# Optimization experiments

Measured on AMD Instinct MI355X. Metric: run time of the kernel, lower is better.

Reference implementation:

```python
import jax, jax.numpy as jnp
import numpy as np

B, C, R, D = 32, 30, 196, 256
K = 20            # max_det_per_class
CONF = 0.5        # conf_threshold
IOU_THR = 0.3     # iou_threshold


def setup_inputs() -> dict:
    key = jax.random.key(0)
    k1, k2, k3 = jax.random.split(key, 3)
    return {
        "local_features": jax.random.normal(k1, (B, C, R, D), dtype=jnp.float32),
        "W_coords": jax.random.normal(k2, (4, D), dtype=jnp.float32) * 0.02,
        "b_coords": jnp.zeros((4,), jnp.float32),
        "W_pres": jax.random.normal(k3, (1, D), dtype=jnp.float32) * 0.02,
        "b_pres": jnp.zeros((1,), jnp.float32),
    }


def _grid_centers_xyxy(num_regions):
    # centers of a GxG grid in normalized coords, repeated to width 4 (xyxy)
    g = int(round(np.sqrt(num_regions)))
    assert g * g == num_regions
    c = (np.arange(g, dtype=np.float32) + 0.5) / g
    cy, cx = np.meshgrid(c, c, indexing="ij")
    centers = np.stack([cx, cy], axis=-1).reshape(-1, 2)  # [R, 2]
    return jnp.asarray(np.tile(centers, (1, 2)))          # [R, 4]


def _pairwise_iou(boxes):
    # boxes: [K, 4] xyxy -> [K, K]
    x1, y1, x2, y2 = boxes[:, 0], boxes[:, 1], boxes[:, 2], boxes[:, 3]
    area = jnp.clip(x2 - x1, 0) * jnp.clip(y2 - y1, 0)
    xx1 = jnp.maximum(x1[:, None], x1[None, :])
    yy1 = jnp.maximum(y1[:, None], y1[None, :])
    xx2 = jnp.minimum(x2[:, None], x2[None, :])
    yy2 = jnp.minimum(y2[:, None], y2[None, :])
    inter = jnp.clip(xx2 - xx1, 0) * jnp.clip(yy2 - yy1, 0)
    union = area[:, None] + area[None, :] - inter
    return inter / jnp.maximum(union, 1e-9)


def _nms_keep(boxes, valid):
    # boxes: [K, 4] already sorted by descending score; valid: [K] bool
    iou = _pairwise_iou(boxes)
    later = jnp.arange(K)

    def body(i, keep):
        sup = keep[i] & (iou[i] > IOU_THR) & (later > i)
        return keep & (~sup)

    return jax.lax.fori_loop(0, K, body, valid)


def _forward(local_features, W_coords, b_coords, W_pres, b_pres):
    # Linear heads: [B, C, R, D] -> [B, C, R, 4] and [B, C, R, 1]
    coords = jnp.einsum("bcrd,od->bcro", local_features, W_coords) + b_coords
    presence = jnp.einsum("bcrd,od->bcro", local_features, W_pres) + b_pres
    probs = jax.nn.sigmoid(presence[..., 0])  # [B, C, R]

    # predict_relative with xyxy format: add grid centers
    coords = coords + _grid_centers_xyxy(R)[None, None]

    # top-k per (image, class); top_k returns scores sorted descending
    probs_k, idx = jax.lax.top_k(probs, K)                      # [B, C, K]
    coords_k = jnp.take_along_axis(coords, idx[..., None], axis=2)  # [B, C, K, 4]

    # confidence threshold (padded mask instead of dynamic shapes)
    valid = probs_k > CONF

    # per-(image, class) greedy NMS; class shift in original => class-separable
    keep = jax.vmap(jax.vmap(_nms_keep))(coords_k, valid)       # [B, C, K] bool
    kf = keep.astype(coords_k.dtype)
    coords_out = coords_k * kf[..., None]
    probs_out = probs_k * kf
    return coords_out, probs_out, keep, presence


def reference(local_features, W_coords, b_coords, W_pres, b_pres):
    return _forward(local_features, W_coords, b_coords, W_pres, b_pres)
```

## Files before the change

kernel.cpp:

```cpp
#include <hip/hip_runtime.h>
#include <hip/hip_bf16.h>
#include <math.h>

#define BB 32
#define CC 30
#define RR 196
#define DD 256
#define KK 20
#define GG 14
#define CONF_ 0.5f
#define IOU_THR_ 0.3f

constexpr int COORDS_OFF = 0;
constexpr int PROBS_OFF  = BB * CC * KK * 4;
constexpr int KEEP_OFF   = PROBS_OFF + BB * CC * KK;
constexpr int PRES_OFF   = KEEP_OFF + BB * CC * KK;

typedef float v4f __attribute__((ext_vector_type(4)));

__device__ __forceinline__ float dot4v(v4f a, v4f b) {
    return a[0] * b[0] + a[1] * b[1] + a[2] * b[2] + a[3] * b[3];
}

#define PIN4(w) asm volatile("" : "+v"(w))

__global__ __launch_bounds__(256, 3) void fused_bbox_fit(
    const v4f*   __restrict__ lf,
    const float* __restrict__ W_coords,
    const float* __restrict__ b_coords,
    const float* __restrict__ W_pres,
    const float* __restrict__ b_pres,
    float* __restrict__ coords_out,
    float* __restrict__ probs_out,
    float* __restrict__ keep_out,
    float* __restrict__ presence_out)
{
    const int bc   = blockIdx.x;
    const int tid  = threadIdx.x;
    const int wv   = tid >> 6;
    const int lane = tid & 63;
    const int gr   = lane >> 4;
    const int o    = lane & 15;

    __shared__ float s_logit[RR];
    __shared__ v4f   s_box[RR];

    const v4f* __restrict__ Wp4 = reinterpret_cast<const v4f*>(W_pres);
    const v4f* __restrict__ Wc4 = reinterpret_cast<const v4f*>(W_coords);

    v4f wp0 = Wp4[o],       wp1 = Wp4[o + 16],      wp2 = Wp4[o + 32],      wp3 = Wp4[o + 48];
    v4f wa0 = Wc4[o],       wa1 = Wc4[o + 16],      wa2 = Wc4[o + 32],      wa3 = Wc4[o + 48];
    v4f wb0 = Wc4[64 + o],  wb1 = Wc4[80 + o],      wb2 = Wc4[96 + o],      wb3 = Wc4[112 + o];
    v4f wc0 = Wc4[128 + o], wc1 = Wc4[144 + o],     wc2 = Wc4[160 + o],     wc3 = Wc4[176 + o];
    v4f wd0 = Wc4[192 + o], wd1 = Wc4[208 + o],     wd2 = Wc4[224 + o],     wd3 = Wc4[240 + o];
    PIN4(wp0); PIN4(wp1); PIN4(wp2); PIN4(wp3);
    PIN4(wa0); PIN4(wa1); PIN4(wa2); PIN4(wa3);
    PIN4(wb0); PIN4(wb1); PIN4(wb2); PIN4(wb3);
    PIN4(wc0); PIN4(wc1); PIN4(wc2); PIN4(wc3);
    PIN4(wd0); PIN4(wd1); PIN4(wd2); PIN4(wd3);

    const float bp  = b_pres[0];
    const float bc0 = b_coords[0], bc1 = b_coords[1];
    const float bc2 = b_coords[2], bc3 = b_coords[3];

    const size_t tile  = (size_t)bc * RR;
    const v4f* __restrict__ tp = lf + tile * 64;
    const int    wbase = wv * 49;

    #pragma unroll 2
    for (int j = 0; j < 12; ++j) {
        const int r = wbase + 4 * j + gr;
        const v4f* __restrict__ rp = tp + (size_t)r * 64;

        const v4f x0 = rp[o];
        const v4f x1 = rp[o + 16];
        const v4f x2 = rp[o + 32];
        const v4f x3 = rp[o + 48];

        float ap = dot4v(x0, wp0) + dot4v(x1, wp1) + dot4v(x2, wp2) + dot4v(x3, wp3);
        float a0 = dot4v(x0, wa0) + dot4v(x1, wa1) + dot4v(x2, wa2) + dot4v(x3, wa3);
        float a1 = dot4v(x0, wb0) + dot4v(x1, wb1) + dot4v(x2, wb2) + dot4v(x3, wb3);
        float a2 = dot4v(x0, wc0) + dot4v(x1, wc1) + dot4v(x2, wc2) + dot4v(x3, wc3);
        float a3 = dot4v(x0, wd0) + dot4v(x1, wd1) + dot4v(x2, wd2) + dot4v(x3, wd3);

        #pragma unroll
        for (int off = 1; off <= 8; off <<= 1) {
            ap += __shfl_xor(ap, off);
            a0 += __shfl_xor(a0, off);
            a1 += __shfl_xor(a1, off);
            a2 += __shfl_xor(a2, off);
            a3 += __shfl_xor(a3, off);
        }
        if (o == 0) {
            const float lg = ap + bp;
            s_logit[r] = lg;
            presence_out[tile + r] = lg;
            const int   ix = r % GG, iy = r / GG;
            const float cx = (ix + 0.5f) / (float)GG;
            const float cy = (iy + 0.5f) / (float)GG;
            v4f b; b[0] = a0 + bc0 + cx; b[1] = a1 + bc1 + cy;
                   b[2] = a2 + bc2 + cx; b[3] = a3 + bc3 + cy;
            s_box[r] = b;
        }
    }

    if (gr == 0) {
        const int r = wbase + 48;
        const v4f* __restrict__ rp = tp + (size_t)r * 64;
        const v4f x0 = rp[o];
        const v4f x1 = rp[o + 16];
        const v4f x2 = rp[o + 32];
        const v4f x3 = rp[o + 48];

        float ap = dot4v(x0, wp0) + dot4v(x1, wp1) + dot4v(x2, wp2) + dot4v(x3, wp3);
        float a0 = dot4v(x0, wa0) + dot4v(x1, wa1) + dot4v(x2, wa2) + dot4v(x3, wa3);
        float a1 = dot4v(x0, wb0) + dot4v(x1, wb1) + dot4v(x2, wb2) + dot4v(x3, wb3);
        float a2 = dot4v(x0, wc0) + dot4v(x1, wc1) + dot4v(x2, wc2) + dot4v(x3, wc3);
        float a3 = dot4v(x0, wd0) + dot4v(x1, wd1) + dot4v(x2, wd2) + dot4v(x3, wd3);

        #pragma unroll
        for (int off = 1; off <= 8; off <<= 1) {
            ap += __shfl_xor(ap, off);
            a0 += __shfl_xor(a0, off);
            a1 += __shfl_xor(a1, off);
            a2 += __shfl_xor(a2, off);
            a3 += __shfl_xor(a3, off);
        }
        if (o == 0) {
            const float lg = ap + bp;
            s_logit[r] = lg;
            presence_out[tile + r] = lg;
            const int   ix = r % GG, iy = r / GG;
            const float cx = (ix + 0.5f) / (float)GG;
            const float cy = (iy + 0.5f) / (float)GG;
            v4f b; b[0] = a0 + bc0 + cx; b[1] = a1 + bc1 + cy;
                   b[2] = a2 + bc2 + cx; b[3] = a3 + bc3 + cy;
            s_box[r] = b;
        }
    }

    __syncthreads();
    if (wv != 0) return;

    float v[4]; int id[4];
    #pragma unroll
    for (int t = 0; t < 4; ++t) {
        const int r = lane + 64 * t;
        id[t] = r;
        v[t]  = (r < RR) ? s_logit[r] : -1e30f;
    }

    float myv = -1e30f; int myi = 0;
    for (int k = 0; k < KK; ++k) {
        float bv = v[0]; int bi = id[0];
        #pragma unroll
        for (int t = 1; t < 4; ++t)
            if (v[t] > bv || (v[t] == bv && id[t] < bi)) { bv = v[t]; bi = id[t]; }
        #pragma unroll
        for (int off = 32; off; off >>= 1) {
            const float ov = __shfl_xor(bv, off);
            const int   oi = __shfl_xor(bi, off);
            if (ov > bv || (ov == bv && oi < bi)) { bv = ov; bi = oi; }
        }
        #pragma unroll
        for (int t = 0; t < 4; ++t)
            if (id[t] == bi) v[t] = -1e30f;
        if (lane == k) { myv = bv; myi = bi; }
    }

    float x1 = 0.f, y1 = 0.f, x2 = 0.f, y2 = 0.f, area = 0.f, prob = 0.f;
    int kp = 0;
    if (lane < KK) {
        const v4f b = s_box[myi];
        x1 = b[0]; y1 = b[1]; x2 = b[2]; y2 = b[3];
        area = fmaxf(x2 - x1, 0.f) * fmaxf(y2 - y1, 0.f);
        prob = 1.f / (1.f + expf(-myv));
        kp   = (prob > CONF_) ? 1 : 0;
    }
    for (int i = 0; i < KK; ++i) {
        const int   ki  = __shfl(kp, i);
        const float bx1 = __shfl(x1, i), by1 = __shfl(y1, i);
        const float bx2 = __shfl(x2, i), by2 = __shfl(y2, i);
        const float ai  = __shfl(area, i);
        if (lane > i && lane < KK && ki) {
            const float xx1 = fmaxf(x1, bx1), yy1 = fmaxf(y1, by1);
            const float xx2 = fminf(x2, bx2), yy2 = fminf(y2, by2);
            const float inter = fmaxf(xx2 - xx1, 0.f) * fmaxf(yy2 - yy1, 0.f);
            const float uni   = area + ai - inter;
            const float iou   = inter / fmaxf(uni, 1e-9f);
            if (iou > IOU_THR_) kp = 0;
        }
    }

    if (lane < KK) {
        const size_t obase = (size_t)bc * KK + lane;
        const float  kf    = kp ? 1.f : 0.f;
        coords_out[obase * 4 + 0] = x1 * kf;
        coords_out[obase * 4 + 1] = y1 * kf;
        coords_out[obase * 4 + 2] = x2 * kf;
        coords_out[obase * 4 + 3] = y2 * kf;
        probs_out[obase] = prob * kf;
        keep_out[obase]  = kf;
    }
}

extern "C" void kernel_launch(void* const* d_in, const int* in_sizes, int n_in,
                              void* d_out, int out_size, void* d_ws, size_t ws_size,
                              hipStream_t stream) {
    const float* lf       = (const float*)d_in[0];
    const float* W_coords = (const float*)d_in[1];
    const float* b_coords = (const float*)d_in[2];
    const float* W_pres   = (const float*)d_in[3];
    const float* b_pres   = (const float*)d_in[4];

    float* out          = (float*)d_out;
    float* coords_out   = out + COORDS_OFF;
    float* probs_out    = out + PROBS_OFF;
    float* keep_out     = out + KEEP_OFF;
    float* presence_out = out + PRES_OFF;

    fused_bbox_fit<<<BB * CC, 256, 0, stream>>>(
        (const v4f*)lf, W_coords, b_coords, W_pres, b_pres,
        coords_out, probs_out, keep_out, presence_out);
}
```

Baseline: 53.64 us.

## Stream feature rows into double-buffered LDS via global_load_lds DMA

Replaces per-thread global vector loads with direct global-to-LDS loads into a two-stage shared buffer of 16 rows, computing the projection from LDS while the next chunk is fetched. Intent is to overlap HBM traffic with the dot-product work and reduce register pressure from in-flight loads. It adds 13 block-wide barriers and extra LDS traffic, and the wait for the async loads may serialize the stages.

```diff
diff --git a/kernel.cpp b/kernel.cpp
--- a/kernel.cpp
+++ b/kernel.cpp
@@ -24,8 +24,8 @@
 
 #define PIN4(w) asm volatile("" : "+v"(w))
 
-__global__ __launch_bounds__(256, 3) void fused_bbox_fit(
-    const v4f*   __restrict__ lf,
+__global__ __launch_bounds__(256, 3) void fused_bbox_dma(
+    const float* __restrict__ lf,
     const float* __restrict__ W_coords,
     const float* __restrict__ b_coords,
     const float* __restrict__ W_pres,
@@ -42,17 +42,18 @@
     const int gr   = lane >> 4;
     const int o    = lane & 15;
 
+    __shared__ v4f   Xb[2][16][64];
     __shared__ float s_logit[RR];
     __shared__ v4f   s_box[RR];
 
     const v4f* __restrict__ Wp4 = reinterpret_cast<const v4f*>(W_pres);
     const v4f* __restrict__ Wc4 = reinterpret_cast<const v4f*>(W_coords);
 
-    v4f wp0 = Wp4[o],       wp1 = Wp4[o + 16],      wp2 = Wp4[o + 32],      wp3 = Wp4[o + 48];
-    v4f wa0 = Wc4[o],       wa1 = Wc4[o + 16],      wa2 = Wc4[o + 32],      wa3 = Wc4[o + 48];
-    v4f wb0 = Wc4[64 + o],  wb1 = Wc4[80 + o],      wb2 = Wc4[96 + o],      wb3 = Wc4[112 + o];
-    v4f wc0 = Wc4[128 + o], wc1 = Wc4[144 + o],     wc2 = Wc4[160 + o],     wc3 = Wc4[176 + o];
-    v4f wd0 = Wc4[192 + o], wd1 = Wc4[208 + o],     wd2 = Wc4[224 + o],     wd3 = Wc4[240 + o];
+    v4f wp0 = Wp4[o],       wp1 = Wp4[o + 16],  wp2 = Wp4[o + 32],  wp3 = Wp4[o + 48];
+    v4f wa0 = Wc4[o],       wa1 = Wc4[o + 16],  wa2 = Wc4[o + 32],  wa3 = Wc4[o + 48];
+    v4f wb0 = Wc4[64 + o],  wb1 = Wc4[80 + o],  wb2 = Wc4[96 + o],  wb3 = Wc4[112 + o];
+    v4f wc0 = Wc4[128 + o], wc1 = Wc4[144 + o], wc2 = Wc4[160 + o], wc3 = Wc4[176 + o];
+    v4f wd0 = Wc4[192 + o], wd1 = Wc4[208 + o], wd2 = Wc4[224 + o], wd3 = Wc4[240 + o];
     PIN4(wp0); PIN4(wp1); PIN4(wp2); PIN4(wp3);
     PIN4(wa0); PIN4(wa1); PIN4(wa2); PIN4(wa3);
     PIN4(wb0); PIN4(wb1); PIN4(wb2); PIN4(wb3);
@@ -63,83 +64,69 @@
     const float bc0 = b_coords[0], bc1 = b_coords[1];
     const float bc2 = b_coords[2], bc3 = b_coords[3];
 
-    const size_t tile  = (size_t)bc * RR;
-    const v4f* __restrict__ tp = lf + tile * 64;
-    const int    wbase = wv * 49;
-
-    #pragma unroll 2
-    for (int j = 0; j < 12; ++j) {
-        const int r = wbase + 4 * j + gr;
-        const v4f* __restrict__ rp = tp + (size_t)r * 64;
-
-        const v4f x0 = rp[o];
-        const v4f x1 = rp[o + 16];
-        const v4f x2 = rp[o + 32];
-        const v4f x3 = rp[o + 48];
-
-        float ap = dot4v(x0, wp0) + dot4v(x1, wp1) + dot4v(x2, wp2) + dot4v(x3, wp3);
-        float a0 = dot4v(x0, wa0) + dot4v(x1, wa1) + dot4v(x2, wa2) + dot4v(x3, wa3);
-        float a1 = dot4v(x0, wb0) + dot4v(x1, wb1) + dot4v(x2, wb2) + dot4v(x3, wb3);
-        float a2 = dot4v(x0, wc0) + dot4v(x1, wc1) + dot4v(x2, wc2) + dot4v(x3, wc3);
-        float a3 = dot4v(x0, wd0) + dot4v(x1, wd1) + dot4v(x2, wd2) + dot4v(x3, wd3);
-
-        #pragma unroll
-        for (int off = 1; off <= 8; off <<= 1) {
-            ap += __shfl_xor(ap, off);
-            a0 += __shfl_xor(a0, off);
-            a1 += __shfl_xor(a1, off);
-            a2 += __shfl_xor(a2, off);
-            a3 += __shfl_xor(a3, off);
-        }
-        if (o == 0) {
-            const float lg = ap + bp;
-            s_logit[r] = lg;
-            presence_out[tile + r] = lg;
-            const int   ix = r % GG, iy = r / GG;
-            const float cx = (ix + 0.5f) / (float)GG;
-            const float cy = (iy + 0.5f) / (float)GG;
-            v4f b; b[0] = a0 + bc0 + cx; b[1] = a1 + bc1 + cy;
-                   b[2] = a2 + bc2 + cx; b[3] = a3 + bc3 + cy;
-            s_box[r] = b;
-        }
-    }
-
-    if (gr == 0) {
-        const int r = wbase + 48;
-        const v4f* __restrict__ rp = tp + (size_t)r * 64;
-        const v4f x0 = rp[o];
-        const v4f x1 = rp[o + 16];
-        const v4f x2 = rp[o + 32];
-        const v4f x3 = rp[o + 48];
-
-        float ap = dot4v(x0, wp0) + dot4v(x1, wp1) + dot4v(x2, wp2) + dot4v(x3, wp3);
-        float a0 = dot4v(x0, wa0) + dot4v(x1, wa1) + dot4v(x2, wa2) + dot4v(x3, wa3);
-        float a1 = dot4v(x0, wb0) + dot4v(x1, wb1) + dot4v(x2, wb2) + dot4v(x3, wb3);
-        float a2 = dot4v(x0, wc0) + dot4v(x1, wc1) + dot4v(x2, wc2) + dot4v(x3, wc3);
-        float a3 = dot4v(x0, wd0) + dot4v(x1, wd1) + dot4v(x2, wd2) + dot4v(x3, wd3);
-
-        #pragma unroll
-        for (int off = 1; off <= 8; off <<= 1) {
-            ap += __shfl_xor(ap, off);
-            a0 += __shfl_xor(a0, off);
-            a1 += __shfl_xor(a1, off);
-            a2 += __shfl_xor(a2, off);
-            a3 += __shfl_xor(a3, off);
-        }
-        if (o == 0) {
-            const float lg = ap + bp;
-            s_logit[r] = lg;
-            presence_out[tile + r] = lg;
-            const int   ix = r % GG, iy = r / GG;
-            const float cx = (ix + 0.5f) / (float)GG;
-            const float cy = (iy + 0.5f) / (float)GG;
-            v4f b; b[0] = a0 + bc0 + cx; b[1] = a1 + bc1 + cy;
-                   b[2] = a2 + bc2 + cx; b[3] = a3 + bc3 + cy;
-            s_box[r] = b;
-        }
-    }
-
+    const size_t tile = (size_t)bc * RR;
+    const char* __restrict__ tbase =
+        reinterpret_cast<const char*>(lf) + tile * (DD * 4);
+
+#define STAGE(c_, b_)                                                        \
+    {                                                                        \
+        _Pragma("unroll")                                                    \
+        for (int i_ = 0; i_ < 4; ++i_) {                                     \
+            int trow_ = 16 * (c_) + 4 * wv + i_;                             \
+            if (trow_ > RR - 1) trow_ = RR - 1;                              \
+            const char* src_ = tbase + (size_t)trow_ * 1024 + (size_t)lane * 16; \
+            __builtin_amdgcn_global_load_lds(                                \
+                (const __attribute__((address_space(1))) void*)src_,         \
+                (__attribute__((address_space(3))) void*)&Xb[b_][4 * wv + i_][0], \
+                16, 0, 0);                                                   \
+        }                                                                    \
+    }
+
+#define COMPUTE(c_, b_)                                                      \
+    {                                                                        \
+        const int jj_ = 4 * wv + gr;                                         \
+        const int r_  = 16 * (c_) + jj_;                                     \
+        if (r_ < RR) {                                                       \
+            const v4f x0 = Xb[b_][jj_][o];                                   \
+            const v4f x1 = Xb[b_][jj_][o + 16];                              \
+            const v4f x2 = Xb[b_][jj_][o + 32];                              \
+            const v4f x3 = Xb[b_][jj_][o + 48];                              \
+            float ap = dot4v(x0, wp0) + dot4v(x1, wp1) + dot4v(x2, wp2) + dot4v(x3, wp3); \
+            float a0 = dot4v(x0, wa0) + dot4v(x1, wa1) + dot4v(x2, wa2) + dot4v(x3, wa3); \
+            float a1 = dot4v(x0, wb0) + dot4v(x1, wb1) + dot4v(x2, wb2) + dot4v(x3, wb3); \
+            float a2 = dot4v(x0, wc0) + dot4v(x1, wc1) + dot4v(x2, wc2) + dot4v(x3, wc3); \
+            float a3 = dot4v(x0, wd0) + dot4v(x1, wd1) + dot4v(x2, wd2) + dot4v(x3, wd3); \
+            _Pragma("unroll")                                                \
+            for (int off_ = 1; off_ <= 8; off_ <<= 1) {                      \
+                ap += __shfl_xor(ap, off_);                                  \
+                a0 += __shfl_xor(a0, off_);                                  \
+                a1 += __shfl_xor(a1, off_);                                  \
+                a2 += __shfl_xor(a2, off_);                                  \
+                a3 += __shfl_xor(a3, off_);                                  \
+            }                                                                \
+            if (o == 0) {                                                    \
+                const float lg_ = ap + bp;                                   \
+                s_logit[r_] = lg_;                                           \
+                presence_out[tile + r_] = lg_;                               \
+                const int   ix_ = r_ % GG, iy_ = r_ / GG;                    \
+                const float cx_ = (ix_ + 0.5f) / (float)GG;                  \
+                const float cy_ = (iy_ + 0.5f) / (float)GG;                  \
+                v4f b__; b__[0] = a0 + bc0 + cx_; b__[1] = a1 + bc1 + cy_;   \
+                         b__[2] = a2 + bc2 + cx_; b__[3] = a3 + bc3 + cy_;   \
+                s_box[r_] = b__;                                             \
+            }                                                                \
+        }                                                                    \
+    }
+
+    STAGE(0, 0);
     __syncthreads();
+    #pragma unroll 1
+    for (int c = 0; c < 13; ++c) {
+        if (c + 1 < 13) STAGE(c + 1, (c + 1) & 1);
+        COMPUTE(c, c & 1);
+        __syncthreads();
+    }
+
     if (wv != 0) return;
 
     float v[4]; int id[4];
@@ -202,6 +189,8 @@
         probs_out[obase] = prob * kf;
         keep_out[obase]  = kf;
     }
+#undef STAGE
+#undef COMPUTE
 }
 
 extern "C" void kernel_launch(void* const* d_in, const int* in_sizes, int n_in,
@@ -219,7 +208,7 @@
     float* keep_out     = out + KEEP_OFF;
     float* presence_out = out + PRES_OFF;
 
-    fused_bbox_fit<<<BB * CC, 256, 0, stream>>>(
-        (const v4f*)lf, W_coords, b_coords, W_pres, b_pres,
+    fused_bbox_dma<<<BB * CC, 256, 0, stream>>>(
+        lf, W_coords, b_coords, W_pres, b_pres,
         coords_out, probs_out, keep_out, presence_out);
 }
```

After: 53.12 us. Within noise of the previous version (-1.0%).
